# Optimization experiments

Measured on AMD Instinct MI355X. Metric: run time of the kernel, lower is better.

Reference implementation:

```python
import jax, jax.numpy as jnp
import numpy as np

D = 1024

def setup_inputs() -> dict:
    key = jax.random.key(0)
    kx, kw = jax.random.split(key)
    x = jax.random.normal(kx, (4, 2048, D), dtype=jnp.float32)
    # nn.Linear(d, 3d, bias=False): weight [3d, d]; y = x @ W.T
    W = jax.random.normal(kw, (3 * D, D), dtype=jnp.float32) * (1.0 / np.sqrt(D))
    return {"x": x, "W": W}

def reference(x, W):
    d = x.shape[-1]
    qkv = jnp.einsum('bsd,ed->bse', x, W)  # [B,S,3d]
    q, k, v = jnp.split(qkv, 3, axis=2)
    att = jnp.einsum('bqd,bkd->bqk', q, k) * (1.0 / jnp.sqrt(jnp.asarray(d, x.dtype)))
    att = jax.nn.softmax(att, axis=-1)
    y = jnp.einsum('bqk,bkd->bqd', att, v)
    return y
```

## Files before the change

kernel.cpp:

```cpp
#include <hip/hip_runtime.h>
#include <hip/hip_bf16.h>

typedef __attribute__((ext_vector_type(8))) short short8;
typedef __attribute__((ext_vector_type(4))) float f32x4;

typedef unsigned short u16;

__device__ __forceinline__ u16 f32_to_bf16(float f) {
    unsigned int u = __float_as_uint(f);
    u += 0x7fffu + ((u >> 16) & 1u);
    return (u16)(u >> 16);
}

__device__ __forceinline__ void gload16(const u16* g, u16* lds_base) {
    __builtin_amdgcn_global_load_lds(
        (const __attribute__((address_space(1))) void*)g,
        (__attribute__((address_space(3))) void*)lds_base, 16, 0, 0);
}

__device__ __forceinline__ void bar() { __builtin_amdgcn_s_barrier(); }
__device__ __forceinline__ void bar_end() {
    __builtin_amdgcn_sched_barrier(0);
    __builtin_amdgcn_s_barrier();
}
__device__ __forceinline__ void wait_vm8() {
    asm volatile("s_waitcnt vmcnt(8)" ::: "memory");
}
__device__ __forceinline__ void wait_vm7() {
    asm volatile("s_waitcnt vmcnt(7)" ::: "memory");
}
__device__ __forceinline__ void wait_vm6() {
    asm volatile("s_waitcnt vmcnt(6)" ::: "memory");
}
__device__ __forceinline__ void wait_vm3() {
    asm volatile("s_waitcnt vmcnt(3)" ::: "memory");
}
__device__ __forceinline__ void wait_vm0() {
    asm volatile("s_waitcnt vmcnt(0)" ::: "memory");
}

__global__ void cast_inputs(const float* __restrict__ x, u16* __restrict__ Xb,
                            const float* __restrict__ W, u16* __restrict__ Wb,
                            float* __restrict__ l,
                            int nx4, int nw4, int nl) {
    int i = blockIdx.x * blockDim.x + threadIdx.x;
    if (i >= nx4 + nw4) {
        int idx = i - (nx4 + nw4);
        if (idx < nl) l[idx] = 0.f;
        return;
    }
    const float* in; u16* out; int idx;
    if (i < nx4) { in = x; out = Xb; idx = i; }
    else { idx = i - nx4; in = W; out = Wb; }
    float4 v = ((const float4*)in)[idx];
    ushort4 o;
    o.x = f32_to_bf16(v.x); o.y = f32_to_bf16(v.y);
    o.z = f32_to_bf16(v.z); o.w = f32_to_bf16(v.w);
    ((ushort4*)out)[idx] = o;
}


struct Acc256 { f32x4 acc[8][4]; };
struct Acc192 { f32x4 acc[8][3]; };
struct Acc128 { f32x4 acc[8][2]; };

template<int MH>
__device__ __forceinline__ void rd_a(const u16* __restrict__ sA, int wr, int lane,
                                     int lr, short8 (&af)[4][2]) {
#pragma unroll
    for (int a2 = 0; a2 < 4; ++a2) {
        const int row = wr * 128 + MH * 64 + a2 * 16 + lr;
#pragma unroll
        for (int k2 = 0; k2 < 2; ++k2) {
            const int cb = (lane >> 4) + k2 * 4;
            af[a2][k2] = *(const short8*)(sA + row * 64 + ((cb ^ (lr & 7)) * 8));
        }
    }
}

template<int NH>
__device__ __forceinline__ void rd_b(const u16* __restrict__ sB, int wc, int lane,
                                     int lr, short8 (&bf)[2][2]) {
#pragma unroll
    for (int b2 = 0; b2 < 2; ++b2) {
        const int row = wc * 64 + NH * 32 + b2 * 16 + lr;
#pragma unroll
        for (int k2 = 0; k2 < 2; ++k2) {
            const int cb = (lane >> 4) + k2 * 4;
            bf[b2][k2] = *(const short8*)(sB + row * 64 + ((cb ^ (lr & 7)) * 8));
        }
    }
}

template<int MH, int NH>
__device__ __forceinline__ void mm_q(Acc256& fr, const short8 (&af)[4][2],
                                     const short8 (&bf)[2][2]) {
    __builtin_amdgcn_s_setprio(1);
#pragma unroll
    for (int a2 = 0; a2 < 4; ++a2)
#pragma unroll
        for (int b2 = 0; b2 < 2; ++b2)
#pragma unroll
            for (int k2 = 0; k2 < 2; ++k2)
                fr.acc[MH * 4 + a2][NH * 2 + b2] =
                    __builtin_amdgcn_mfma_f32_16x16x32_bf16(
                        af[a2][k2], bf[b2][k2],
                        fr.acc[MH * 4 + a2][NH * 2 + b2], 0, 0, 0);
    __builtin_amdgcn_s_setprio(0);
}

__device__ __forceinline__ void rd_b01(const u16* __restrict__ sB, int wc, int lane,
                                       int lr, short8 (&bf)[2][2]) {
#pragma unroll
    for (int b2 = 0; b2 < 2; ++b2) {
        const int row = wc * 48 + b2 * 16 + lr;
#pragma unroll
        for (int k2 = 0; k2 < 2; ++k2) {
            const int cb = (lane >> 4) + k2 * 4;
            bf[b2][k2] = *(const short8*)(sB + row * 64 + ((cb ^ (lr & 7)) * 8));
        }
    }
}

__device__ __forceinline__ void rd_b2(const u16* __restrict__ sB, int wc, int lane,
                                      int lr, short8 (&bf)[2]) {
    const int row = wc * 48 + 32 + lr;
#pragma unroll
    for (int k2 = 0; k2 < 2; ++k2) {
        const int cb = (lane >> 4) + k2 * 4;
        bf[k2] = *(const short8*)(sB + row * 64 + ((cb ^ (lr & 7)) * 8));
    }
}

template<int MH>
__device__ __forceinline__ void mm_b01(Acc192& fr, const short8 (&af)[4][2],
                                       const short8 (&bf)[2][2]) {
    __builtin_amdgcn_s_setprio(1);
#pragma unroll
    for (int a2 = 0; a2 < 4; ++a2)
#pragma unroll
        for (int b2 = 0; b2 < 2; ++b2)
#pragma unroll
            for (int k2 = 0; k2 < 2; ++k2)
                fr.acc[MH * 4 + a2][b2] =
                    __builtin_amdgcn_mfma_f32_16x16x32_bf16(
                        af[a2][k2], bf[b2][k2],
                        fr.acc[MH * 4 + a2][b2], 0, 0, 0);
    __builtin_amdgcn_s_setprio(0);
}

template<int MH>
__device__ __forceinline__ void mm_b2(Acc192& fr, const short8 (&af)[4][2],
                                      const short8 (&bf)[2]) {
    __builtin_amdgcn_s_setprio(1);
#pragma unroll
    for (int a2 = 0; a2 < 4; ++a2)
#pragma unroll
        for (int k2 = 0; k2 < 2; ++k2)
            fr.acc[MH * 4 + a2][2] =
                __builtin_amdgcn_mfma_f32_16x16x32_bf16(
                    af[a2][k2], bf[k2], fr.acc[MH * 4 + a2][2], 0, 0, 0);
    __builtin_amdgcn_s_setprio(0);
}

__device__ __forceinline__ void rd_bb(const u16* __restrict__ sB, int wc, int lane,
                                      int lr, short8 (&bf)[2][2]) {
#pragma unroll
    for (int b2 = 0; b2 < 2; ++b2) {
        const int row = wc * 32 + b2 * 16 + lr;
#pragma unroll
        for (int k2 = 0; k2 < 2; ++k2) {
            const int cb = (lane >> 4) + k2 * 4;
            bf[b2][k2] = *(const short8*)(sB + row * 64 + ((cb ^ (lr & 7)) * 8));
        }
    }
}

template<int MH>
__device__ __forceinline__ void mm_n128(Acc128& fr, const short8 (&af)[4][2],
                                        const short8 (&bf)[2][2]) {
    __builtin_amdgcn_s_setprio(1);
#pragma unroll
    for (int a2 = 0; a2 < 4; ++a2)
#pragma unroll
        for (int b2 = 0; b2 < 2; ++b2)
#pragma unroll
            for (int k2 = 0; k2 < 2; ++k2)
                fr.acc[MH * 4 + a2][b2] =
                    __builtin_amdgcn_mfma_f32_16x16x32_bf16(
                        af[a2][k2], bf[b2][k2],
                        fr.acc[MH * 4 + a2][b2], 0, 0, 0);
    __builtin_amdgcn_s_setprio(0);
}

__device__ __forceinline__ void gemm_core_256(
    const u16* __restrict__ A, const u16* __restrict__ Bt,
    int K, int lda, int ldb, int row0, int col0, u16* sm, Acc256& fr)
{
    const int t    = threadIdx.x;
    const int lane = t & 63;
    const int wave = t >> 6;
    const int wr   = wave >> 2;
    const int wc   = wave & 3;
    const int lr   = lane & 15;
    const int srow = lane >> 3;
    const int gc   = (lane & 7) ^ srow;

    const u16* const sA0 = sm;
    const u16* const sA1 = sm + 16384;
    const u16* const sB0 = sm + 32768;
    const u16* const sB1 = sm + 49152;

#pragma unroll
    for (int a = 0; a < 8; ++a)
#pragma unroll
        for (int b = 0; b < 4; ++b)
            fr.acc[a][b] = (f32x4){0.f, 0.f, 0.f, 0.f};

    const u16* aB = A  + (long long)(row0 + wave * 8 + srow) * lda + gc * 8;
    const u16* bB = Bt + (long long)(col0 + wave * 8 + srow) * ldb + gc * 8;
    u16* const sAw = sm + wave * 512;
    u16* const sBw = sm + 32768 + wave * 512;

    auto stageA = [&](int kt) {
        u16* d = sAw + (kt & 1) * 16384;
        const u16* g = aB + kt * 64;
#pragma unroll
        for (int r4 = 0; r4 < 4; ++r4)
            gload16(g + (long long)(r4 * 64) * lda, d + r4 * 4096);
    };
    auto stageB = [&](int kt) {
        u16* d = sBw + (kt & 1) * 16384;
        const u16* g = bB + kt * 64;
#pragma unroll
        for (int r4 = 0; r4 < 4; ++r4)
            gload16(g + (long long)(r4 * 64) * ldb, d + r4 * 4096);
    };

    stageA(0); stageB(0); stageA(1); stageB(1);
    wait_vm8();
    bar();

    const int NI = K >> 7;
    short8 af[4][2], bfa[2][2], bfb[2][2];
#pragma unroll 1
    for (int i = 0; i < NI; ++i) {
        const bool more = (i + 1 < NI);
        const int t2 = 2 * i + 2;

        rd_a<0>(sA0, wr, lane, lr, af);
        rd_b<0>(sB0, wc, lane, lr, bfa);
        bar();
        mm_q<0, 0>(fr, af, bfa);
        bar_end();

        rd_b<1>(sB0, wc, lane, lr, bfb);
        bar();
        mm_q<0, 1>(fr, af, bfb);
        bar_end();

        rd_a<1>(sA0, wr, lane, lr, af);
        if (more) stageB(t2);
        bar();
        mm_q<1, 1>(fr, af, bfb);
        bar_end();

        if (more) stageA(t2);
        bar();
        mm_q<1, 0>(fr, af, bfa);
        if (more) wait_vm8(); else wait_vm0();
        bar_end();

        rd_a<0>(sA1, wr, lane, lr, af);
        rd_b<0>(sB1, wc, lane, lr, bfa);
        bar();
        mm_q<0, 0>(fr, af, bfa);
        bar_end();

        rd_b<1>(sB1, wc, lane, lr, bfb);
        bar();
        mm_q<0, 1>(fr, af, bfb);
        bar_end();

        rd_a<1>(sA1, wr, lane, lr, af);
        if (more) stageB(t2 + 1);
        bar();
        mm_q<1, 1>(fr, af, bfb);
        bar_end();

        if (more) stageA(t2 + 1);
        bar();
        mm_q<1, 0>(fr, af, bfa);
        if (more) wait_vm8();
        bar_end();
    }
}

__device__ __forceinline__ void gemm_core_192(
    const u16* __restrict__ A, const u16* __restrict__ Bt,
    int K, int lda, int ldb, int row0, int col0, u16* sm, Acc192& fr)
{
    const int t    = threadIdx.x;
    const int lane = t & 63;
    const int wave = t >> 6;
    const int wr   = wave >> 2;
    const int wc   = wave & 3;
    const int lr   = lane & 15;
    const int srow = lane >> 3;
    const int gc   = (lane & 7) ^ srow;

    const u16* const sA0 = sm;
    const u16* const sA1 = sm + 16384;
    const u16* const sB0 = sm + 32768;
    const u16* const sB1 = sm + 45056;

#pragma unroll
    for (int a = 0; a < 8; ++a)
#pragma unroll
        for (int b = 0; b < 3; ++b)
            fr.acc[a][b] = (f32x4){0.f, 0.f, 0.f, 0.f};

    const u16* aB = A  + (long long)(row0 + wave * 8 + srow) * lda + gc * 8;
    const u16* bB = Bt + (long long)(col0 + wave * 8 + srow) * ldb + gc * 8;
    u16* const sAw = sm + wave * 512;
    u16* const sBw = sm + 32768 + wave * 512;

    auto stageA = [&](int kt) {
        u16* d = sAw + (kt & 1) * 16384;
        const u16* g = aB + kt * 64;
#pragma unroll
        for (int r4 = 0; r4 < 4; ++r4)
            gload16(g + (long long)(r4 * 64) * lda, d + r4 * 4096);
    };
    auto stageB = [&](int kt) {
        u16* d = sBw + (kt & 1) * 12288;
        const u16* g = bB + kt * 64;
#pragma unroll
        for (int r4 = 0; r4 < 3; ++r4)
            gload16(g + (long long)(r4 * 64) * ldb, d + r4 * 4096);
    };

    stageA(0); stageB(0); stageA(1); stageB(1);
    wait_vm7();
    bar();

    short8 afP[4][2], afQ[4][2], bfaP[2][2], bfaQ[2][2], bfb[2];
    rd_a<0>(sA0, wr, lane, lr, afP);
    rd_b01(sB0, wc, lane, lr, bfaP);

    const int NT = K >> 6;
#pragma unroll 1
    for (int i = 0; i < NT; i += 2) {
        const bool more = (i + 2 < NT);

        rd_b2(sB0, wc, lane, lr, bfb);
        mm_b01<0>(fr, afP, bfaP);
        bar();

        rd_a<1>(sA0, wr, lane, lr, afQ);
        mm_b2<0>(fr, afP, bfb);
        bar();

        mm_b2<1>(fr, afQ, bfb);
        __builtin_amdgcn_sched_barrier(0);
        if (more) { stageB(i + 2); wait_vm3(); } else wait_vm0();
        bar();

        rd_a<0>(sA1, wr, lane, lr, afP);
        rd_b01(sB1, wc, lane, lr, bfaQ);
        mm_b01<1>(fr, afQ, bfaP);
        __builtin_amdgcn_sched_barrier(0);
        if (more) stageA(i + 2);
        bar();

        rd_b2(sB1, wc, lane, lr, bfb);
        mm_b01<0>(fr, afP, bfaQ);
        bar();

        rd_a<1>(sA1, wr, lane, lr, afQ);
        mm_b2<0>(fr, afP, bfb);
        bar();

        mm_b2<1>(fr, afQ, bfb);
        __builtin_amdgcn_sched_barrier(0);
        if (more) { stageB(i + 3); wait_vm3(); } else wait_vm0();
        bar();

        if (more) {
            rd_a<0>(sA0, wr, lane, lr, afP);
            rd_b01(sB0, wc, lane, lr, bfaP);
        }
        mm_b01<1>(fr, afQ, bfaQ);
        __builtin_amdgcn_sched_barrier(0);
        if (more) stageA(i + 3);
        bar();
    }
}

__device__ __forceinline__ void gemm_core_n128(
    const u16* __restrict__ A, const u16* __restrict__ Bt,
    int K, int lda, int ldb, int row0, int col0, u16* sm, Acc128& fr)
{
    const int t    = threadIdx.x;
    const int lane = t & 63;
    const int wave = t >> 6;
    const int wr   = wave >> 2;
    const int wc   = wave & 3;
    const int lr   = lane & 15;
    const int srow = lane >> 3;
    const int gc   = (lane & 7) ^ srow;

    const u16* const sA0 = sm;
    const u16* const sA1 = sm + 16384;
    const u16* const sB0 = sm + 32768;
    const u16* const sB1 = sm + 40960;

#pragma unroll
    for (int a = 0; a < 8; ++a)
#pragma unroll
        for (int b = 0; b < 2; ++b)
            fr.acc[a][b] = (f32x4){0.f, 0.f, 0.f, 0.f};

    const u16* aB = A  + (long long)(row0 + wave * 8 + srow) * lda + gc * 8;
    const u16* bB = Bt + (long long)(col0 + wave * 8 + srow) * ldb + gc * 8;
    u16* const sAw = sm + wave * 512;
    u16* const sBw = sm + 32768 + wave * 512;

    auto stageA = [&](int kt) {
        u16* d = sAw + (kt & 1) * 16384;
        const u16* g = aB + kt * 64;
#pragma unroll
        for (int r4 = 0; r4 < 4; ++r4)
            gload16(g + (long long)(r4 * 64) * lda, d + r4 * 4096);
    };
    auto stageB = [&](int kt) {
        u16* d = sBw + (kt & 1) * 8192;
        const u16* g = bB + kt * 64;
#pragma unroll
        for (int r4 = 0; r4 < 2; ++r4)
            gload16(g + (long long)(r4 * 64) * ldb, d + r4 * 4096);
    };

    stageB(0); stageA(0); stageB(1); stageA(1);
    wait_vm6();
    bar();

    const int NI = K >> 7;
    short8 af[4][2], bf[2][2];
#pragma unroll 1
    for (int i = 0; i < NI; ++i) {
        const bool more = (i + 1 < NI);
        const int t2 = 2 * i + 2;

        rd_a<0>(sA0, wr, lane, lr, af);
        rd_bb(sB0, wc, lane, lr, bf);
        if (more) stageB(t2);
        bar();
        mm_n128<0>(fr, af, bf);
        bar_end();

        rd_a<1>(sA0, wr, lane, lr, af);
        if (more) stageA(t2);
        bar();
        mm_n128<1>(fr, af, bf);
        if (more) wait_vm6(); else wait_vm0();
        bar_end();

        rd_a<0>(sA1, wr, lane, lr, af);
        rd_bb(sB1, wc, lane, lr, bf);
        if (more) stageB(t2 + 1);
        bar();
        mm_n128<0>(fr, af, bf);
        bar_end();

        rd_a<1>(sA1, wr, lane, lr, af);
        if (more) stageA(t2 + 1);
        bar();
        mm_n128<1>(fr, af, bf);
        if (more) wait_vm6();
        bar_end();
    }
}


__global__ __launch_bounds__(512, 1) void gemm_qkv(
    const u16* __restrict__ Xb, const u16* __restrict__ Wb,
    u16* __restrict__ QK, u16* __restrict__ VT)
{
    __shared__ u16 sm[57344];
    const int row0 = blockIdx.y * 256;
    const int col0 = blockIdx.x * 192;

    Acc192 fr;
    gemm_core_192(Xb, Wb, 1024, 1024, 1024, row0, col0, sm, fr);

    const int lane = threadIdx.x & 63;
    const int wave = threadIdx.x >> 6;
    const int wr = wave >> 2, wc = wave & 3;
    const int cr = (lane >> 4) * 4, cc = lane & 15;

#pragma unroll
    for (int a = 0; a < 8; ++a) {
        const int grow = row0 + wr * 128 + a * 16 + cr;
#pragma unroll
        for (int b = 0; b < 3; ++b) {
            const int gcol = col0 + wc * 48 + b * 16 + cc;
            if (gcol < 2048) {
#pragma unroll
                for (int r = 0; r < 4; ++r)
                    QK[(long long)(grow + r) * 2048 + gcol] =
                        f32_to_bf16(fr.acc[a][b][r]);
            } else {
                const int bz = grow >> 11, s = grow & 2047;
                const int d = gcol - 2048;
                ushort4 o;
                o.x = f32_to_bf16(fr.acc[a][b][0]);
                o.y = f32_to_bf16(fr.acc[a][b][1]);
                o.z = f32_to_bf16(fr.acc[a][b][2]);
                o.w = f32_to_bf16(fr.acc[a][b][3]);
                *(ushort4*)(&VT[((long long)(bz * 1024 + d)) * 2048 + s]) = o;
            }
        }
    }
}

__global__ __launch_bounds__(512, 1) void gemm_s_exp(
    const u16* __restrict__ QK, u16* __restrict__ E, float* __restrict__ l)
{
    __shared__ u16 sm[65536];
    const long long boff = (long long)blockIdx.z * 2048 * 2048;
    const u16* Q  = QK + boff;
    const u16* Kp = QK + boff + 1024;
    u16* Eb = E + boff;
    float* lb = l + (long long)blockIdx.z * 2048;
    const int row0 = blockIdx.y * 256;
    const int col0 = blockIdx.x * 256;

    Acc256 fr;
    gemm_core_256(Q, Kp, 1024, 2048, 2048, row0, col0, sm, fr);

    const int lane = threadIdx.x & 63;
    const int wave = threadIdx.x >> 6;
    const int wr = wave >> 2, wc = wave & 3;
    const int cr = (lane >> 4) * 4, cc = lane & 15;

#pragma unroll
    for (int a = 0; a < 8; ++a) {
        float rs[4] = {0.f, 0.f, 0.f, 0.f};
#pragma unroll
        for (int b = 0; b < 4; ++b)
#pragma unroll
            for (int r = 0; r < 4; ++r) {
                float e = __expf(fr.acc[a][b][r] * 0.03125f);
                rs[r] += e;
                int grow = row0 + wr * 128 + a * 16 + cr + r;
                int gcol = col0 + wc * 64 + b * 16 + cc;
                Eb[(long long)grow * 2048 + gcol] = f32_to_bf16(e);
            }
#pragma unroll
        for (int r = 0; r < 4; ++r) {
#pragma unroll
            for (int m = 1; m < 16; m <<= 1) rs[r] += __shfl_xor(rs[r], m, 64);
            if ((lane & 15) == 0)
                atomicAdd(&lb[row0 + wr * 128 + a * 16 + cr + r], rs[r]);
        }
    }
}

__global__ __launch_bounds__(512, 1) void gemm_pv(
    const u16* __restrict__ E, const u16* __restrict__ VT,
    const float* __restrict__ l, float* __restrict__ Y)
{
    __shared__ u16 sm[49152];
    const u16* Eb  = E  + (long long)blockIdx.z * 2048 * 2048;
    const u16* VTb = VT + (long long)blockIdx.z * 1024 * 2048;
    const float* lb = l + (long long)blockIdx.z * 2048;
    float* Yb = Y + (long long)blockIdx.z * 2048 * 1024;
    const int row0 = blockIdx.x * 256;
    const int col0 = blockIdx.y * 128;

    Acc128 fr;
    gemm_core_n128(Eb, VTb, 2048, 2048, 2048, row0, col0, sm, fr);

    const int lane = threadIdx.x & 63;
    const int wave = threadIdx.x >> 6;
    const int wr = wave >> 2, wc = wave & 3;
    const int cr = (lane >> 4) * 4, cc = lane & 15;

#pragma unroll
    for (int a = 0; a < 8; ++a) {
        const int q0 = row0 + wr * 128 + a * 16 + cr;
        const float4 l4 = *(const float4*)(&lb[q0]);
        const float inv0 = 1.0f / l4.x, inv1 = 1.0f / l4.y;
        const float inv2 = 1.0f / l4.z, inv3 = 1.0f / l4.w;
#pragma unroll
        for (int b = 0; b < 2; ++b) {
            const int d = col0 + wc * 32 + b * 16 + cc;
            Yb[(long long)(q0 + 0) * 1024 + d] = fr.acc[a][b][0] * inv0;
            Yb[(long long)(q0 + 1) * 1024 + d] = fr.acc[a][b][1] * inv1;
            Yb[(long long)(q0 + 2) * 1024 + d] = fr.acc[a][b][2] * inv2;
            Yb[(long long)(q0 + 3) * 1024 + d] = fr.acc[a][b][3] * inv3;
        }
    }
}

extern "C" void kernel_launch(void* const* d_in, const int* in_sizes, int n_in,
                              void* d_out, int out_size, void* d_ws, size_t ws_size,
                              hipStream_t stream) {
    const float* x = (const float*)d_in[0];
    const float* W = (const float*)d_in[1];
    float* out = (float*)d_out;

    char* ws = (char*)d_ws;
    u16*   Xb = (u16*)(ws);
    u16*   Wb = (u16*)(ws + 16777216LL);
    u16*   QK = (u16*)(ws + 23068672LL);
    u16*   VT = (u16*)(ws + 56623104LL);
    u16*   E  = (u16*)(ws + 73400320LL);
    float* l  = (float*)(ws + 106954752LL);

    const int nx4 = 8192 * 1024 / 4, nw4 = 3072 * 1024 / 4;
    cast_inputs<<<11296, 256, 0, stream>>>(x, Xb, W, Wb, l, nx4, nw4, 8192);
    gemm_qkv<<<dim3(16, 32, 1), 512, 0, stream>>>(Xb, Wb, QK, VT);
    gemm_s_exp<<<dim3(8, 8, 4), 512, 0, stream>>>(QK, E, l);
    gemm_pv<<<dim3(8, 8, 4), 512, 0, stream>>>(E, VT, l, out);
}
```

Measured before the change: 226.0 us.

## Software-pipeline LDS fragment reads with MFMA using double-buffered register fragments

```diff
diff --git a/kernel.cpp b/kernel.cpp
--- a/kernel.cpp
+++ b/kernel.cpp
@@ -1,5 +1,6 @@
 #include <hip/hip_runtime.h>
 #include <hip/hip_bf16.h>
+
 
 typedef __attribute__((ext_vector_type(8))) short short8;
 typedef __attribute__((ext_vector_type(4))) float f32x4;
@@ -31,6 +32,9 @@
 }
 __device__ __forceinline__ void wait_vm6() {
     asm volatile("s_waitcnt vmcnt(6)" ::: "memory");
+}
+__device__ __forceinline__ void wait_vm4() {
+    asm volatile("s_waitcnt vmcnt(4)" ::: "memory");
 }
 __device__ __forceinline__ void wait_vm3() {
     asm volatile("s_waitcnt vmcnt(3)" ::: "memory");
@@ -241,58 +245,56 @@
     wait_vm8();
     bar();
 
-    const int NI = K >> 7;
-    short8 af[4][2], bfa[2][2], bfb[2][2];
+    short8 afP[4][2], afQ[4][2], bfaP[2][2], bfaQ[2][2], bfb[2][2];
+    rd_a<0>(sA0, wr, lane, lr, afP);
+    rd_b<0>(sB0, wc, lane, lr, bfaP);
+
+    const int NT = K >> 6;
 #pragma unroll 1
-    for (int i = 0; i < NI; ++i) {
-        const bool more = (i + 1 < NI);
-        const int t2 = 2 * i + 2;
-
-        rd_a<0>(sA0, wr, lane, lr, af);
-        rd_b<0>(sB0, wc, lane, lr, bfa);
-        bar();
-        mm_q<0, 0>(fr, af, bfa);
-        bar_end();
+    for (int i = 0; i < NT; i += 2) {
+        const bool more = (i + 2 < NT);
 
         rd_b<1>(sB0, wc, lane, lr, bfb);
-        bar();
-        mm_q<0, 1>(fr, af, bfb);
-        bar_end();
-
-        rd_a<1>(sA0, wr, lane, lr, af);
-        if (more) stageB(t2);
-        bar();
-        mm_q<1, 1>(fr, af, bfb);
-        bar_end();
-
-        if (more) stageA(t2);
-        bar();
-        mm_q<1, 0>(fr, af, bfa);
-        if (more) wait_vm8(); else wait_vm0();
-        bar_end();
-
-        rd_a<0>(sA1, wr, lane, lr, af);
-        rd_b<0>(sB1, wc, lane, lr, bfa);
-        bar();
-        mm_q<0, 0>(fr, af, bfa);
-        bar_end();
+        mm_q<0, 0>(fr, afP, bfaP);
+        bar();
+
+        rd_a<1>(sA0, wr, lane, lr, afQ);
+        mm_q<0, 1>(fr, afP, bfb);
+        bar();
+
+        mm_q<1, 1>(fr, afQ, bfb);
+        __builtin_amdgcn_sched_barrier(0);
+        if (more) { stageB(i + 2); wait_vm4(); } else wait_vm0();
+        bar();
+
+        rd_a<0>(sA1, wr, lane, lr, afP);
+        rd_b<0>(sB1, wc, lane, lr, bfaQ);
+        mm_q<1, 0>(fr, afQ, bfaP);
+        __builtin_amdgcn_sched_barrier(0);
+        if (more) stageA(i + 2);
+        bar();
 
         rd_b<1>(sB1, wc, lane, lr, bfb);
-        bar();
-        mm_q<0, 1>(fr, af, bfb);
-        bar_end();
-
-        rd_a<1>(sA1, wr, lane, lr, af);
-        if (more) stageB(t2 + 1);
-        bar();
-        mm_q<1, 1>(fr, af, bfb);
-        bar_end();
-
-        if (more) stageA(t2 + 1);
-        bar();
-        mm_q<1, 0>(fr, af, bfa);
-        if (more) wait_vm8();
-        bar_end();
+        mm_q<0, 0>(fr, afP, bfaQ);
+        bar();
+
+        rd_a<1>(sA1, wr, lane, lr, afQ);
+        mm_q<0, 1>(fr, afP, bfb);
+        bar();
+
+        mm_q<1, 1>(fr, afQ, bfb);
+        __builtin_amdgcn_sched_barrier(0);
+        if (more) { stageB(i + 3); wait_vm4(); } else wait_vm0();
+        bar();
+
+        if (more) {
+            rd_a<0>(sA0, wr, lane, lr, afP);
+            rd_b<0>(sB0, wc, lane, lr, bfaP);
+        }
+        mm_q<1, 0>(fr, afQ, bfaQ);
+        __builtin_amdgcn_sched_barrier(0);
+        if (more) stageA(i + 3);
+        bar();
     }
 }
 
```

Result: slower. 239.5 us (+5.9%).

## Software-pipeline LDS fragment reads with MFMA in the 128-wide GEMM core

Applied to the files above, without the earlier changes.

```diff
diff --git a/kernel.cpp b/kernel.cpp
--- a/kernel.cpp
+++ b/kernel.cpp
@@ -1,5 +1,6 @@
 #include <hip/hip_runtime.h>
 #include <hip/hip_bf16.h>
+
 
 typedef __attribute__((ext_vector_type(8))) short short8;
 typedef __attribute__((ext_vector_type(4))) float f32x4;
@@ -34,6 +35,9 @@
 }
 __device__ __forceinline__ void wait_vm3() {
     asm volatile("s_waitcnt vmcnt(3)" ::: "memory");
+}
+__device__ __forceinline__ void wait_vm2() {
+    asm volatile("s_waitcnt vmcnt(2)" ::: "memory");
 }
 __device__ __forceinline__ void wait_vm0() {
     asm volatile("s_waitcnt vmcnt(0)" ::: "memory");
@@ -163,33 +167,28 @@
     __builtin_amdgcn_s_setprio(0);
 }
 
-__device__ __forceinline__ void rd_bb(const u16* __restrict__ sB, int wc, int lane,
-                                      int lr, short8 (&bf)[2][2]) {
-#pragma unroll
-    for (int b2 = 0; b2 < 2; ++b2) {
-        const int row = wc * 32 + b2 * 16 + lr;
-#pragma unroll
-        for (int k2 = 0; k2 < 2; ++k2) {
-            const int cb = (lane >> 4) + k2 * 4;
-            bf[b2][k2] = *(const short8*)(sB + row * 64 + ((cb ^ (lr & 7)) * 8));
-        }
-    }
-}
-
-template<int MH>
-__device__ __forceinline__ void mm_n128(Acc128& fr, const short8 (&af)[4][2],
-                                        const short8 (&bf)[2][2]) {
+template<int BI>
+__device__ __forceinline__ void rd_b1f(const u16* __restrict__ sB, int wc, int lane,
+                                       int lr, short8 (&bf)[2]) {
+    const int row = wc * 32 + BI * 16 + lr;
+#pragma unroll
+    for (int k2 = 0; k2 < 2; ++k2) {
+        const int cb = (lane >> 4) + k2 * 4;
+        bf[k2] = *(const short8*)(sB + row * 64 + ((cb ^ (lr & 7)) * 8));
+    }
+}
+
+template<int MH, int BI>
+__device__ __forceinline__ void mm_h(Acc128& fr, const short8 (&af)[4][2],
+                                     const short8 (&bf)[2]) {
     __builtin_amdgcn_s_setprio(1);
 #pragma unroll
     for (int a2 = 0; a2 < 4; ++a2)
 #pragma unroll
-        for (int b2 = 0; b2 < 2; ++b2)
-#pragma unroll
-            for (int k2 = 0; k2 < 2; ++k2)
-                fr.acc[MH * 4 + a2][b2] =
-                    __builtin_amdgcn_mfma_f32_16x16x32_bf16(
-                        af[a2][k2], bf[b2][k2],
-                        fr.acc[MH * 4 + a2][b2], 0, 0, 0);
+        for (int k2 = 0; k2 < 2; ++k2)
+            fr.acc[MH * 4 + a2][BI] =
+                __builtin_amdgcn_mfma_f32_16x16x32_bf16(
+                    af[a2][k2], bf[k2], fr.acc[MH * 4 + a2][BI], 0, 0, 0);
     __builtin_amdgcn_s_setprio(0);
 }
 
@@ -445,40 +444,56 @@
     wait_vm6();
     bar();
 
-    const int NI = K >> 7;
-    short8 af[4][2], bf[2][2];
+    short8 afP[4][2], afQ[4][2], b0P[2], b0Q[2], bfb[2];
+    rd_a<0>(sA0, wr, lane, lr, afP);
+    rd_b1f<0>(sB0, wc, lane, lr, b0P);
+
+    const int NT = K >> 6;
 #pragma unroll 1
-    for (int i = 0; i < NI; ++i) {
-        const bool more = (i + 1 < NI);
-        const int t2 = 2 * i + 2;
-
-        rd_a<0>(sA0, wr, lane, lr, af);
-        rd_bb(sB0, wc, lane, lr, bf);
-        if (more) stageB(t2);
-        bar();
-        mm_n128<0>(fr, af, bf);
-        bar_end();
-
-        rd_a<1>(sA0, wr, lane, lr, af);
-        if (more) stageA(t2);
-        bar();
-        mm_n128<1>(fr, af, bf);
-        if (more) wait_vm6(); else wait_vm0();
-        bar_end();
-
-        rd_a<0>(sA1, wr, lane, lr, af);
-        rd_bb(sB1, wc, lane, lr, bf);
-        if (more) stageB(t2 + 1);
-        bar();
-        mm_n128<0>(fr, af, bf);
-        bar_end();
-
-        rd_a<1>(sA1, wr, lane, lr, af);
-        if (more) stageA(t2 + 1);
-        bar();
-        mm_n128<1>(fr, af, bf);
-        if (more) wait_vm6();
-        bar_end();
+    for (int i = 0; i < NT; i += 2) {
+        const bool more = (i + 2 < NT);
+
+        rd_b1f<1>(sB0, wc, lane, lr, bfb);
+        mm_h<0, 0>(fr, afP, b0P);
+        bar();
+
+        rd_a<1>(sA0, wr, lane, lr, afQ);
+        mm_h<0, 1>(fr, afP, bfb);
+        bar();
+
+        mm_h<1, 1>(fr, afQ, bfb);
+        __builtin_amdgcn_sched_barrier(0);
+        if (more) { stageB(i + 2); wait_vm2(); } else wait_vm0();
+        bar();
+
+        rd_a<0>(sA1, wr, lane, lr, afP);
+        rd_b1f<0>(sB1, wc, lane, lr, b0Q);
+        mm_h<1, 0>(fr, afQ, b0P);
+        __builtin_amdgcn_sched_barrier(0);
+        if (more) stageA(i + 2);
+        bar();
+
+        rd_b1f<1>(sB1, wc, lane, lr, bfb);
+        mm_h<0, 0>(fr, afP, b0Q);
+        bar();
+
+        rd_a<1>(sA1, wr, lane, lr, afQ);
+        mm_h<0, 1>(fr, afP, bfb);
+        bar();
+
+        mm_h<1, 1>(fr, afQ, bfb);
+        __builtin_amdgcn_sched_barrier(0);
+        if (more) { stageB(i + 3); wait_vm2(); } else wait_vm0();
+        bar();
+
+        if (more) {
+            rd_a<0>(sA0, wr, lane, lr, afP);
+            rd_b1f<0>(sB0, wc, lane, lr, b0P);
+        }
+        mm_h<1, 0>(fr, afQ, b0Q);
+        __builtin_amdgcn_sched_barrier(0);
+        if (more) stageA(i + 3);
+        bar();
     }
 }
 
```

Result: no change. 226.8 us (+0.3%).
